# Performance work log

Hardware: AMD Instinct MI355X
Metric: run time of the kernel (lower is better)

The kernel has to match this reference:

```python
import jax, jax.numpy as jnp
import numpy as np

N_LIG, M_POC = 16384, 32768
E_LIG, E_POC, K_CROSS = 163840, 327680, 8
H = 64
L = 4

silu = jax.nn.silu


def _lin(k, fan_in, fan_out):
    k1, k2 = jax.random.split(k)
    s = 1.0 / np.sqrt(fan_in)
    W = jax.random.uniform(k1, (fan_in, fan_out), jnp.float32, -s, s)
    b = jax.random.uniform(k2, (fan_out,), jnp.float32, -s, s)
    return W, b


def setup_inputs() -> dict:
    key = jax.random.key(0)
    ks = jax.random.split(key, 32)
    inp = {
        'lig_x': jax.random.normal(ks[0], (N_LIG, 3), jnp.float32),
        'lig_h': jax.random.normal(ks[1], (N_LIG, 17), jnp.float32),
        'poc_x': jax.random.normal(ks[2], (M_POC, 3), jnp.float32),
        'poc_h': jax.random.normal(ks[3], (M_POC, 29), jnp.float32),
        'lig_edge_index': jax.random.randint(ks[4], (2, E_LIG), 0, N_LIG, jnp.int32),
        'lig_edge_attr': jax.random.normal(ks[5], (E_LIG, 6), jnp.float32),
        'poc_edge_index': jax.random.randint(ks[6], (2, E_POC), 0, M_POC, jnp.int32),
        'poc_edge_attr': jax.random.normal(ks[7], (E_POC, 16), jnp.float32),
        'cross_edge_index': jnp.stack([
            jax.random.randint(ks[8], (N_LIG * K_CROSS,), 0, M_POC, jnp.int32),
            jax.random.randint(ks[9], (N_LIG * K_CROSS,), 0, N_LIG, jnp.int32)]),
        'cross_edge_attr': jax.random.normal(ks[10], (N_LIG * K_CROSS, 16), jnp.float32),
        't': jax.random.uniform(ks[11], (1,), jnp.float32),
    }
    # embeddings
    inp['lig_emb_W'], inp['lig_emb_b'] = _lin(ks[12], 18, H)
    inp['poc_emb_W'], inp['poc_emb_b'] = _lin(ks[13], 29, H)
    inp['lig_ee_W'], inp['lig_ee_b'] = _lin(ks[14], 6, H)
    inp['poc_ee_W'], inp['poc_ee_b'] = _lin(ks[15], 16, H)
    inp['cross_ee_W'], inp['cross_ee_b'] = _lin(ks[16], 16, H)
    # per-layer params stacked along leading L axis
    def stack(kk, fan_in, fan_out):
        Ws, bs = zip(*[_lin(k, fan_in, fan_out) for k in jax.random.split(kk, L)])
        return jnp.stack(Ws), jnp.stack(bs)
    inp['phi_e_W1'], inp['phi_e_b1'] = stack(ks[17], 2 * H + 1 + H, H)
    inp['phi_e_W2'], inp['phi_e_b2'] = stack(ks[18], H, H)
    inp['phi_x_W1'], inp['phi_x_b1'] = stack(ks[19], H, H)
    inp['phi_x_W2'], inp['phi_x_b2'] = stack(ks[20], H, 1)
    inp['phi_h_W1'], inp['phi_h_b1'] = stack(ks[21], 2 * H, H)
    inp['phi_h_W2'], inp['phi_h_b2'] = stack(ks[22], H, H)
    inp['out_W1'], inp['out_b1'] = _lin(ks[23], H, H)
    inp['out_W2'], inp['out_b2'] = _lin(ks[24], H, 1)
    return inp


def _forward(lig_x, lig_h, poc_x, poc_h, lig_edge_attr, poc_edge_attr,
             cross_edge_attr, t,
             lig_emb_W, lig_emb_b, poc_emb_W, poc_emb_b,
             lig_ee_W, lig_ee_b, poc_ee_W, poc_ee_b, cross_ee_W, cross_ee_b,
             phi_e_W1, phi_e_b1, phi_e_W2, phi_e_b2,
             phi_x_W1, phi_x_b1, phi_x_W2, phi_x_b2,
             phi_h_W1, phi_h_b1, phi_h_W2, phi_h_b2,
             out_W1, out_b1, out_W2, out_b2,
             lig_edge_index, poc_edge_index, cross_edge_index):
    n_lig = lig_h.shape[0]
    n_tot = n_lig + poc_h.shape[0]
    t_feat = jnp.broadcast_to(t.reshape(1, 1), (n_lig, 1))
    h_lig = jnp.concatenate([lig_h, t_feat], -1) @ lig_emb_W + lig_emb_b
    h_poc = poc_h @ poc_emb_W + poc_emb_b
    h = jnp.concatenate([h_lig, h_poc], 0)          # [N, H]
    x = jnp.concatenate([lig_x, poc_x], 0)          # [N, 3]
    src = jnp.concatenate([lig_edge_index[0], poc_edge_index[0] + n_lig,
                           cross_edge_index[0] + n_lig])
    dst = jnp.concatenate([lig_edge_index[1], poc_edge_index[1] + n_lig,
                           cross_edge_index[1]])
    eattr = jnp.concatenate([
        lig_edge_attr @ lig_ee_W + lig_ee_b,
        poc_edge_attr @ poc_ee_W + poc_ee_b,
        cross_edge_attr @ cross_ee_W + cross_ee_b], 0)  # [E, H]
    # True = pocket => coords not updated
    update_mask = jnp.concatenate([
        jnp.ones((n_lig, 1), h.dtype), jnp.zeros((n_tot - n_lig, 1), h.dtype)], 0)
    for i in range(phi_e_W1.shape[0]):
        diff = x[src] - x[dst]                                    # [E, 3]
        dist = jnp.sum(diff * diff, -1, keepdims=True) / 100.0    # [E, 1]
        e_in = jnp.concatenate([h[src], h[dst], dist, eattr], -1) # [E, 2H+1+H]
        m = silu(silu(e_in @ phi_e_W1[i] + phi_e_b1[i]) @ phi_e_W2[i] + phi_e_b2[i])
        cw = jnp.tanh(silu(m @ phi_x_W1[i] + phi_x_b1[i]) @ phi_x_W2[i] + phi_x_b2[i])
        coord_agg = jax.ops.segment_sum(diff * cw, dst, num_segments=n_tot) * update_mask
        msg_agg = jax.ops.segment_sum(m, dst, num_segments=n_tot)
        h = h + silu(jnp.concatenate([h, msg_agg], -1) @ phi_h_W1[i] + phi_h_b1[i]) @ phi_h_W2[i] + phi_h_b2[i]
        x = x + coord_agg
    disp = x[:n_lig] - lig_x
    scale = silu(h[:n_lig] @ out_W1 + out_b1) @ out_W2 + out_b2
    return scale * disp


def reference(lig_x, lig_h, poc_x, poc_h, lig_edge_attr, poc_edge_attr,
              cross_edge_attr, t,
              lig_emb_W, lig_emb_b, poc_emb_W, poc_emb_b,
              lig_ee_W, lig_ee_b, poc_ee_W, poc_ee_b, cross_ee_W, cross_ee_b,
              phi_e_W1, phi_e_b1, phi_e_W2, phi_e_b2,
              phi_x_W1, phi_x_b1, phi_x_W2, phi_x_b2,
              phi_h_W1, phi_h_b1, phi_h_W2, phi_h_b2,
              out_W1, out_b1, out_W2, out_b2,
              lig_edge_index, poc_edge_index, cross_edge_index):
    return _forward(lig_x, lig_h, poc_x, poc_h, lig_edge_attr, poc_edge_attr,
                    cross_edge_attr, t,
                    lig_emb_W, lig_emb_b, poc_emb_W, poc_emb_b,
                    lig_ee_W, lig_ee_b, poc_ee_W, poc_ee_b, cross_ee_W, cross_ee_b,
                    phi_e_W1, phi_e_b1, phi_e_W2, phi_e_b2,
                    phi_x_W1, phi_x_b1, phi_x_W2, phi_x_b2,
                    phi_h_W1, phi_h_b1, phi_h_W2, phi_h_b2,
                    out_W1, out_b1, out_W2, out_b2,
                    lig_edge_index, poc_edge_index, cross_edge_index)
```

## Files before the change

### kernel.cpp

```cpp
#include <hip/hip_runtime.h>

#define N_LIG 16384
#define M_POC 32768
#define N_TOT (N_LIG + M_POC)
#define E_LIG 163840
#define E_POC 327680
#define E_CROSS (N_LIG * 8)
#define E_TOT (E_LIG + E_POC + E_CROSS)
#define TE 16

typedef __bf16 bf16_t;
typedef bf16_t bf16x8 __attribute__((ext_vector_type(8)));
typedef bf16_t bf16x4 __attribute__((ext_vector_type(4)));
typedef bf16_t bf16x2 __attribute__((ext_vector_type(2)));
typedef float f32x4 __attribute__((ext_vector_type(4)));

#define S1 168
#define S2 72
#define WAVE_BYTES 7936

__device__ __forceinline__ float silu_f(float v) { return v / (1.0f + __expf(-v)); }

__device__ __forceinline__ float tanh_f(float v) {
    float a = fabsf(v);
    float t = __expf(-2.0f * a);
    float r = (1.0f - t) / (1.0f + t);
    return copysignf(r, v);
}

__device__ __forceinline__ void atomic_add_f32(float* p, float v) {
    __hip_atomic_fetch_add(p, v, __ATOMIC_RELAXED, __HIP_MEMORY_SCOPE_AGENT);
}


__global__ void k_build_edges(const int* __restrict__ lig_ei, const int* __restrict__ poc_ei,
                              const int* __restrict__ cross_ei,
                              int* __restrict__ srcA, int* __restrict__ dstA,
                              int* __restrict__ cnt) {
    int e = blockIdx.x * blockDim.x + threadIdx.x;
    if (e < N_TOT) cnt[e] = 0;
    if (e >= E_TOT) return;
    int s, d;
    if (e < E_LIG) {
        s = lig_ei[e];
        d = lig_ei[E_LIG + e];
    } else if (e < E_LIG + E_POC) {
        int i = e - E_LIG;
        s = poc_ei[i] + N_LIG;
        d = poc_ei[E_POC + i] + N_LIG;
    } else {
        int i = e - E_LIG - E_POC;
        s = cross_ei[i] + N_LIG;
        d = cross_ei[E_CROSS + i];
    }
    srcA[e] = s;
    dstA[e] = d;
}

__global__ void k_hist(const int* __restrict__ dstA, int* __restrict__ cnt) {
    int e = blockIdx.x * blockDim.x + threadIdx.x;
    if (e < E_TOT) atomicAdd(&cnt[dstA[e]], 1);
}

__global__ __launch_bounds__(1024) void k_scan(const int* __restrict__ cnt,
                                               int* __restrict__ rowptr,
                                               int* __restrict__ cursor) {
    __shared__ int sums[1024];
    int tid = threadIdx.x;
    int local[48];
    int s = 0;
    for (int i = 0; i < 48; ++i) { local[i] = s; s += cnt[tid * 48 + i]; }
    sums[tid] = s;
    __syncthreads();
    for (int off = 1; off < 1024; off <<= 1) {
        int v = (tid >= off) ? sums[tid - off] : 0;
        __syncthreads();
        sums[tid] += v;
        __syncthreads();
    }
    int base = (tid == 0) ? 0 : sums[tid - 1];
    for (int i = 0; i < 48; ++i) {
        int v = base + local[i];
        int idx = tid * 48 + i;
        rowptr[idx] = v;
        cursor[idx] = v;
    }
    if (tid == 1023) rowptr[N_TOT] = sums[1023];
}

__global__ void k_scatter(const int* __restrict__ dstA, int* __restrict__ cursor,
                          int* __restrict__ sortedPos) {
    int e = blockIdx.x * blockDim.x + threadIdx.x;
    if (e < E_TOT) sortedPos[e] = atomicAdd(&cursor[dstA[e]], 1);
}

#define PK_G1   (12 * 5 * 4 * 64)
#define PK_G23  (4 * 4 * 4 * 64)
#define PK_WP   (4 * 48 * 256)
#define PK_BEFF (12 * 64)
#define PK_TOT  (PK_G1 + PK_G23 + PK_WP + PK_BEFF)

__global__ void k_pack_all(const float* __restrict__ phi_e_W1, const float* __restrict__ phi_e_b1,
                           const float* __restrict__ lig_ee_W, const float* __restrict__ lig_ee_b,
                           const float* __restrict__ poc_ee_W, const float* __restrict__ poc_ee_b,
                           const float* __restrict__ cross_ee_W, const float* __restrict__ cross_ee_b,
                           const float* __restrict__ phi_e_W2, const float* __restrict__ phi_x_W1,
                           const float* __restrict__ phi_h_W1, const float* __restrict__ phi_h_W2,
                           bf16_t* __restrict__ Bg1, bf16_t* __restrict__ Bg23,
                           float* __restrict__ Wp, float* __restrict__ beff) {
    int tid = blockIdx.x * blockDim.x + threadIdx.x;
    if (tid < PK_G1) {
        int lt = tid / 1280;
        int rem = tid - lt * 1280;
        int c = rem >> 8;
        int nt = (rem >> 6) & 3;
        int lane = rem & 63;
        int l = lt / 3, t = lt % 3;
        const float* W1l = phi_e_W1 + l * 193 * 64;
        const float* We; int K;
        if (t == 0) { We = lig_ee_W; K = 6; }
        else if (t == 1) { We = poc_ee_W; K = 16; }
        else { We = cross_ee_W; K = 16; }
        int col = nt * 16 + (lane & 15);
        int k0 = c * 32 + (lane >> 4) * 8;
        #pragma unroll
        for (int j = 0; j < 8; ++j) {
            int row = k0 + j;
            float v = 0.0f;
            if (row < 129) v = W1l[row * 64 + col];
            else if (row >= 132 && row < 132 + K) {
                int kk = row - 132;
                float a = 0.0f;
                for (int q = 0; q < 64; ++q) a = fmaf(We[kk * 64 + q], W1l[(129 + q) * 64 + col], a);
                v = a;
            }
            Bg1[(size_t)tid * 8 + j] = (bf16_t)v;
        }
    } else if (tid < PK_G1 + PK_G23) {
        int u = tid - PK_G1;
        int lane = u & 63;
        int nt = (u >> 6) & 3;
        int c = (u >> 8) & 3;
        int l = u >> 10;
        const float* W = (c < 2) ? (phi_e_W2 + l * 4096) : (phi_x_W1 + l * 4096);
        int kb = (c & 1) * 32;
        int col = nt * 16 + (lane & 15);
        int k0 = kb + (lane >> 4) * 8;
        #pragma unroll
        for (int j = 0; j < 8; ++j)
            Bg23[(size_t)u * 8 + j] = (bf16_t)W[(k0 + j) * 64 + col];
    } else if (tid < PK_G1 + PK_G23 + PK_WP) {
        int idx = tid - PK_G1 - PK_G23;
        int l = idx / (48 * 256);
        int rem = idx - l * (48 * 256);
        int c = rem / 256;
        int q = rem - c * 256;
        int j = q >> 2;
        int kk = q & 3;
        const float* W; int Ksrc; int k4;
        if (c < 32) { W = phi_h_W1 + l * 128 * 64; Ksrc = 128; k4 = c; }
        else        { W = phi_h_W2 + l * 64 * 64;  Ksrc = 64;  k4 = c - 32; }
        int k = k4 * 4 + kk;
        Wp[idx] = (k < Ksrc) ? W[k * 64 + j] : 0.0f;
    } else if (tid < PK_TOT) {
        int u = tid - PK_G1 - PK_G23 - PK_WP;
        int j = u & 63;
        int lt = u >> 6;
        int l = lt / 3, t = lt % 3;
        const float* W1l = phi_e_W1 + l * 193 * 64;
        const float* Be = (t == 0) ? lig_ee_b : ((t == 1) ? poc_ee_b : cross_ee_b);
        float v = phi_e_b1[l * 64 + j];
        for (int q = 0; q < 64; ++q) v = fmaf(Be[q], W1l[(129 + q) * 64 + j], v);
        beff[u] = v;
    }
}

__global__ void k_embed(const float* __restrict__ lig_x, const float* __restrict__ lig_h,
                        const float* __restrict__ poc_x, const float* __restrict__ poc_h,
                        const float* __restrict__ t,
                        const float* __restrict__ ligW, const float* __restrict__ ligB,
                        const float* __restrict__ pocW, const float* __restrict__ pocB,
                        float* __restrict__ h, bf16_t* __restrict__ hB, float* __restrict__ x) {
    int gid = blockIdx.x * blockDim.x + threadIdx.x;
    int n = gid >> 6;
    int lane = gid & 63;
    if (n >= N_TOT) return;
    float a;
    if (n < N_LIG) {
        a = ligB[lane];
        #pragma unroll
        for (int k = 0; k < 17; ++k) a = fmaf(lig_h[n * 17 + k], ligW[k * 64 + lane], a);
        a = fmaf(t[0], ligW[17 * 64 + lane], a);
        if (lane < 3) x[n * 3 + lane] = lig_x[n * 3 + lane];
    } else {
        int p = n - N_LIG;
        a = pocB[lane];
        #pragma unroll
        for (int k = 0; k < 29; ++k) a = fmaf(poc_h[p * 29 + k], pocW[k * 64 + lane], a);
        if (lane < 3) x[n * 3 + lane] = poc_x[p * 3 + lane];
    }
    h[n * 64 + lane] = a;
    hB[n * 64 + lane] = (bf16_t)a;
}

__global__ __launch_bounds__(256) void k_edge_mfma(
    const bf16_t* __restrict__ hB, const float* __restrict__ x,
    const int* __restrict__ srcA, const int* __restrict__ dstA,
    const int* __restrict__ sortedPos,
    const float* __restrict__ lig_attr, const float* __restrict__ poc_attr,
    const float* __restrict__ cross_attr,
    const bf16_t* __restrict__ Bg1L,
    const float* __restrict__ beffL,
    const bf16_t* __restrict__ Bg23L,
    const float* __restrict__ b2, const float* __restrict__ bx1,
    const float* __restrict__ Wx2, const float* __restrict__ bx2,
    bf16_t* __restrict__ mBuf, float* __restrict__ coord_agg) {
    __shared__ __align__(16) char lds[4 * WAVE_BYTES];
    const int lane = threadIdx.x & 63;
    const int wave = threadIdx.x >> 6;
    bf16_t* einA = (bf16_t*)(lds + wave * WAVE_BYTES);
    bf16_t* mA   = (bf16_t*)(lds + wave * WAVE_BYTES + 5376);
    float*  dfL  = (float*)(lds + wave * WAVE_BYTES + 5376 + 2304);
    const int base = (blockIdx.x * 4 + wave) * TE;

    int t; const float* attrBase;
    if (base < E_LIG) { t = 0; attrBase = lig_attr + (size_t)base * 6; }
    else if (base < E_LIG + E_POC) { t = 1; attrBase = poc_attr + (size_t)(base - E_LIG) * 16; }
    else { t = 2; attrBase = cross_attr + (size_t)(base - E_LIG - E_POC) * 16; }

    const int e16 = base + (lane & 15);
    const int sv = srcA[e16];
    const int dv = dstA[e16];
    const int sp = sortedPos[e16];

    {
        bf16x8 z = {(bf16_t)0.f, (bf16_t)0.f, (bf16_t)0.f, (bf16_t)0.f,
                    (bf16_t)0.f, (bf16_t)0.f, (bf16_t)0.f, (bf16_t)0.f};
        *(bf16x8*)(einA + (lane >> 2) * S1 + 128 + (lane & 3) * 8) = z;
    }

    #pragma unroll
    for (int i = 0; i < 4; ++i) {
        const int row = i * 4 + (lane >> 4);
        const int s = __shfl(sv, row, 64);
        const int d = __shfl(dv, row, 64);
        bf16x4 hs = *(const bf16x4*)(hB + (size_t)s * 64 + (lane & 15) * 4);
        bf16x4 hd = *(const bf16x4*)(hB + (size_t)d * 64 + (lane & 15) * 4);
        *(bf16x4*)(einA + row * S1 + (lane & 15) * 4) = hs;
        *(bf16x4*)(einA + row * S1 + 64 + (lane & 15) * 4) = hd;
    }

    if (lane < 16) {
        const float* xs = x + (size_t)sv * 3;
        const float* xd = x + (size_t)dv * 3;
        float d0 = xs[0] - xd[0];
        float d1 = xs[1] - xd[1];
        float d2 = xs[2] - xd[2];
        float dist = (d0 * d0 + d1 * d1 + d2 * d2) * 0.01f;
        einA[lane * S1 + 128] = (bf16_t)dist;
        *(float4*)(dfL + lane * 4) = (float4){d0, d1, d2, dist};
    }

    {
        const int r = lane >> 2, q = lane & 3;
        if (t == 0) {
            if (q < 3) {
                float2 a = *(const float2*)(attrBase + r * 6 + q * 2);
                bf16x2 av = {(bf16_t)a.x, (bf16_t)a.y};
                *(bf16x2*)(einA + r * S1 + 132 + q * 2) = av;
            }
        } else {
            float4 a = *(const float4*)(attrBase + r * 16 + q * 4);
            bf16x4 av = {(bf16_t)a.x, (bf16_t)a.y, (bf16_t)a.z, (bf16_t)a.w};
            *(bf16x4*)(einA + r * S1 + 132 + q * 4) = av;
        }
    }
    __syncthreads();

    const int mcol = lane & 15;
    const int mrow0 = (lane >> 4) * 4;
    const int kgrp = lane >> 4;

    const bf16_t* Bg1 = Bg1L + (size_t)t * 5 * 4 * 512;
    const float* beff = beffL + t * 64;
    f32x4 acc1[4];
    #pragma unroll
    for (int nt = 0; nt < 4; ++nt) {
        float bv = beff[nt * 16 + mcol];
        acc1[nt] = (f32x4){bv, bv, bv, bv};
    }
    const bf16_t* aBase = einA + mcol * S1 + kgrp * 8;
    #pragma unroll
    for (int c = 0; c < 5; ++c) {
        bf16x8 af = *(const bf16x8*)(aBase + c * 32);
        #pragma unroll
        for (int nt = 0; nt < 4; ++nt) {
            bf16x8 bfr = *(const bf16x8*)(Bg1 + ((size_t)(c * 4 + nt) * 64 + lane) * 8);
            acc1[nt] = __builtin_amdgcn_mfma_f32_16x16x32_bf16(af, bfr, acc1[nt], 0, 0, 0);
        }
    }
    __syncthreads();
    #pragma unroll
    for (int nt = 0; nt < 4; ++nt)
        #pragma unroll
        for (int g = 0; g < 4; ++g)
            mA[(mrow0 + g) * S2 + nt * 16 + mcol] = (bf16_t)silu_f(acc1[nt][g]);
    __syncthreads();

    f32x4 acc2[4];
    #pragma unroll
    for (int nt = 0; nt < 4; ++nt) {
        float bv = b2[nt * 16 + mcol];
        acc2[nt] = (f32x4){bv, bv, bv, bv};
    }
    const bf16_t* aBase2 = mA + mcol * S2 + kgrp * 8;
    #pragma unroll
    for (int c = 0; c < 2; ++c) {
        bf16x8 af = *(const bf16x8*)(aBase2 + c * 32);
        #pragma unroll
        for (int nt = 0; nt < 4; ++nt) {
            bf16x8 bfr = *(const bf16x8*)(Bg23L + ((size_t)(c * 4 + nt) * 64 + lane) * 8);
            acc2[nt] = __builtin_amdgcn_mfma_f32_16x16x32_bf16(af, bfr, acc2[nt], 0, 0, 0);
        }
    }
    __syncthreads();
    #pragma unroll
    for (int nt = 0; nt < 4; ++nt)
        #pragma unroll
        for (int g = 0; g < 4; ++g)
            mA[(mrow0 + g) * S2 + nt * 16 + mcol] = (bf16_t)silu_f(acc2[nt][g]);
    __syncthreads();

    #pragma unroll
    for (int p = 0; p < 2; ++p) {
        const int r = p * 8 + (lane >> 3);
        const int c8 = (lane & 7) * 8;
        bf16x8 mrow = *(const bf16x8*)(mA + r * S2 + c8);
        const int pos = __shfl(sp, r, 64);
        *(bf16x8*)(mBuf + (size_t)pos * 64 + c8) = mrow;
    }

    f32x4 acc3[4];
    #pragma unroll
    for (int nt = 0; nt < 4; ++nt) {
        float bv = bx1[nt * 16 + mcol];
        acc3[nt] = (f32x4){bv, bv, bv, bv};
    }
    const bf16_t* Bg3 = Bg23L + (size_t)2 * 4 * 512;
    #pragma unroll
    for (int c = 0; c < 2; ++c) {
        bf16x8 af = *(const bf16x8*)(aBase2 + c * 32);
        #pragma unroll
        for (int nt = 0; nt < 4; ++nt) {
            bf16x8 bfr = *(const bf16x8*)(Bg3 + ((size_t)(c * 4 + nt) * 64 + lane) * 8);
            acc3[nt] = __builtin_amdgcn_mfma_f32_16x16x32_bf16(af, bfr, acc3[nt], 0, 0, 0);
        }
    }

    const float bx2v = bx2[0];
    float s[4] = {0.f, 0.f, 0.f, 0.f};
    #pragma unroll
    for (int nt = 0; nt < 4; ++nt) {
        float w = Wx2[nt * 16 + mcol];
        #pragma unroll
        for (int g = 0; g < 4; ++g) s[g] = fmaf(silu_f(acc3[nt][g]), w, s[g]);
    }
    #pragma unroll
    for (int g = 0; g < 4; ++g) {
        float p = s[g];
        #pragma unroll
        for (int off = 1; off < 16; off <<= 1) p += __shfl_xor(p, off, 64);
        const float cw = tanh_f(p + bx2v);
        const int d = __shfl(dv, mrow0 + g, 64);
        if (d < N_LIG && mcol < 3)
            atomic_add_f32(&coord_agg[d * 3 + mcol], dfL[(mrow0 + g) * 4 + mcol] * cw);
    }
}

__global__ __launch_bounds__(256) void k_node(
    float* __restrict__ h, bf16_t* __restrict__ hB, float* __restrict__ x,
    const bf16_t* __restrict__ mBuf, const int* __restrict__ rowptr,
    float* __restrict__ coord,
    const float* __restrict__ Wh1p, const float* __restrict__ bh1,
    const float* __restrict__ Wh2p, const float* __restrict__ bh2) {
    __shared__ __align__(16) float lds[4][TE * 128];
    const int lane = threadIdx.x & 63;
    const int wave = threadIdx.x >> 6;
    float* inL = lds[wave];
    const int base = (blockIdx.x * 4 + wave) * TE;

    #pragma unroll
    for (int i = 0; i < 4; ++i) {
        int fidx = i * 256 + lane * 4;
        float4 v = *(const float4*)(h + (size_t)base * 64 + fidx);
        *(float4*)(inL + (fidx >> 6) * 128 + (fidx & 63)) = v;
    }

    const int n16 = base + (lane & 15);
    const int rp0 = rowptr[n16];
    const int rp1 = rowptr[n16 + 1];
    const int sub = lane >> 4;
    const int f4 = (lane & 15) * 4;
    for (int r = 0; r < TE; ++r) {
        const int s0 = __shfl(rp0, r, 64);
        const int s1 = __shfl(rp1, r, 64);
        float a0 = 0.f, a1 = 0.f, a2 = 0.f, a3 = 0.f;
        for (int i = s0 + sub; i < s1; i += 4) {
            bf16x4 v = *(const bf16x4*)(mBuf + (size_t)i * 64 + f4);
            a0 += (float)v[0]; a1 += (float)v[1]; a2 += (float)v[2]; a3 += (float)v[3];
        }
        a0 += __shfl_xor(a0, 16, 64); a1 += __shfl_xor(a1, 16, 64);
        a2 += __shfl_xor(a2, 16, 64); a3 += __shfl_xor(a3, 16, 64);
        a0 += __shfl_xor(a0, 32, 64); a1 += __shfl_xor(a1, 32, 64);
        a2 += __shfl_xor(a2, 32, 64); a3 += __shfl_xor(a3, 32, 64);
        if (lane < 16)
            *(float4*)(inL + r * 128 + 64 + f4) = (float4){a0, a1, a2, a3};
    }
    __syncthreads();

    float acc[TE];
    #pragma unroll
    for (int r = 0; r < TE; ++r) acc[r] = bh1[lane];
    for (int c = 0; c < 32; ++c) {
        const float4 w = *(const float4*)(Wh1p + (c * 64 + lane) * 4);
        #pragma unroll
        for (int r = 0; r < TE; ++r) {
            const float4 v = *(const float4*)(inL + r * 128 + c * 4);
            acc[r] = fmaf(v.x, w.x, fmaf(v.y, w.y, fmaf(v.z, w.z, fmaf(v.w, w.w, acc[r]))));
        }
    }
    __syncthreads();
    #pragma unroll
    for (int r = 0; r < TE; ++r) inL[r * 64 + lane] = silu_f(acc[r]);
    __syncthreads();

    float acc2[TE];
    #pragma unroll
    for (int r = 0; r < TE; ++r) acc2[r] = bh2[lane];
    for (int c = 0; c < 16; ++c) {
        const float4 w = *(const float4*)(Wh2p + (c * 64 + lane) * 4);
        #pragma unroll
        for (int r = 0; r < TE; ++r) {
            const float4 v = *(const float4*)(inL + r * 64 + c * 4);
            acc2[r] = fmaf(v.x, w.x, fmaf(v.y, w.y, fmaf(v.z, w.z, fmaf(v.w, w.w, acc2[r]))));
        }
    }
    for (int r = 0; r < TE; ++r) {
        const int n = base + r;
        float hv = h[n * 64 + lane] + acc2[r];
        h[n * 64 + lane] = hv;
        hB[n * 64 + lane] = (bf16_t)hv;
        if (lane < 3) {
            if (n < N_LIG) x[n * 3 + lane] += coord[n * 3 + lane];
            coord[n * 3 + lane] = 0.0f;
        }
    }
}

__global__ void k_out(const float* __restrict__ h, const float* __restrict__ x,
                      const float* __restrict__ lig_x,
                      const float* __restrict__ oW1, const float* __restrict__ ob1,
                      const float* __restrict__ oW2, const float* __restrict__ ob2,
                      float* __restrict__ out) {
    int gid = blockIdx.x * blockDim.x + threadIdx.x;
    int n = gid >> 6;
    int lane = gid & 63;
    if (n >= N_LIG) return;
    float hv = h[n * 64 + lane];
    float a = ob1[lane];
    #pragma unroll
    for (int k = 0; k < 64; ++k) a = fmaf(__shfl(hv, k, 64), oW1[k * 64 + lane], a);
    float p = silu_f(a) * oW2[lane];
    #pragma unroll
    for (int off = 32; off > 0; off >>= 1) p += __shfl_xor(p, off, 64);
    float scale = p + ob2[0];
    if (lane < 3) out[n * 3 + lane] = scale * (x[n * 3 + lane] - lig_x[n * 3 + lane]);
}

extern "C" void kernel_launch(void* const* d_in, const int* in_sizes, int n_in,
                              void* d_out, int out_size, void* d_ws, size_t ws_size,
                              hipStream_t stream) {
    const float* lig_x      = (const float*)d_in[0];
    const float* lig_h      = (const float*)d_in[1];
    const float* poc_x      = (const float*)d_in[2];
    const float* poc_h      = (const float*)d_in[3];
    const int*   lig_ei     = (const int*)d_in[4];
    const float* lig_attr   = (const float*)d_in[5];
    const int*   poc_ei     = (const int*)d_in[6];
    const float* poc_attr   = (const float*)d_in[7];
    const int*   cross_ei   = (const int*)d_in[8];
    const float* cross_attr = (const float*)d_in[9];
    const float* t          = (const float*)d_in[10];
    const float* lig_emb_W  = (const float*)d_in[11];
    const float* lig_emb_b  = (const float*)d_in[12];
    const float* poc_emb_W  = (const float*)d_in[13];
    const float* poc_emb_b  = (const float*)d_in[14];
    const float* lig_ee_W   = (const float*)d_in[15];
    const float* lig_ee_b   = (const float*)d_in[16];
    const float* poc_ee_W   = (const float*)d_in[17];
    const float* poc_ee_b   = (const float*)d_in[18];
    const float* cross_ee_W = (const float*)d_in[19];
    const float* cross_ee_b = (const float*)d_in[20];
    const float* phi_e_W1   = (const float*)d_in[21];
    const float* phi_e_b1   = (const float*)d_in[22];
    const float* phi_e_W2   = (const float*)d_in[23];
    const float* phi_e_b2   = (const float*)d_in[24];
    const float* phi_x_W1   = (const float*)d_in[25];
    const float* phi_x_b1   = (const float*)d_in[26];
    const float* phi_x_W2   = (const float*)d_in[27];
    const float* phi_x_b2   = (const float*)d_in[28];
    const float* phi_h_W1   = (const float*)d_in[29];
    const float* phi_h_b1   = (const float*)d_in[30];
    const float* phi_h_W2   = (const float*)d_in[31];
    const float* phi_h_b2   = (const float*)d_in[32];
    const float* out_W1     = (const float*)d_in[33];
    const float* out_b1     = (const float*)d_in[34];
    const float* out_W2     = (const float*)d_in[35];
    const float* out_b2     = (const float*)d_in[36];

    char* p = (char*)d_ws;
    auto carve = [&](size_t bytes) { char* r = p; p += (bytes + 255) & ~(size_t)255; return r; };
    float*  h      = (float*)carve((size_t)N_TOT * 64 * 4);
    bf16_t* hB     = (bf16_t*)carve((size_t)N_TOT * 64 * 2);
    float*  xx     = (float*)carve((size_t)N_TOT * 3 * 4);
    float*  coord  = (float*)carve((size_t)N_TOT * 3 * 4);
    float*  Wp     = (float*)carve((size_t)4 * 48 * 256 * 4);
    float*  beff   = (float*)carve((size_t)12 * 64 * 4);
    bf16_t* Bg1    = (bf16_t*)carve((size_t)12 * 5 * 4 * 512 * 2);
    bf16_t* Bg23   = (bf16_t*)carve((size_t)4 * 16 * 512 * 2);
    int*    srcA   = (int*)carve((size_t)E_TOT * 4);
    int*    dstA   = (int*)carve((size_t)E_TOT * 4);
    int*    sortedPos = (int*)carve((size_t)E_TOT * 4);
    int*    cnt    = (int*)carve((size_t)N_TOT * 4);
    int*    cursor = (int*)carve((size_t)N_TOT * 4);
    int*    rowptr = (int*)carve((size_t)(N_TOT + 1) * 4);
    bf16_t* mBuf   = (bf16_t*)carve((size_t)E_TOT * 64 * 2);

    k_build_edges<<<E_TOT / 256, 256, 0, stream>>>(lig_ei, poc_ei, cross_ei, srcA, dstA, cnt);
    k_hist<<<E_TOT / 256, 256, 0, stream>>>(dstA, cnt);
    k_scan<<<1, 1024, 0, stream>>>(cnt, rowptr, cursor);
    k_scatter<<<E_TOT / 256, 256, 0, stream>>>(dstA, cursor, sortedPos);
    k_pack_all<<<(PK_TOT + 255) / 256, 256, 0, stream>>>(
        phi_e_W1, phi_e_b1, lig_ee_W, lig_ee_b, poc_ee_W, poc_ee_b, cross_ee_W, cross_ee_b,
        phi_e_W2, phi_x_W1, phi_h_W1, phi_h_W2, Bg1, Bg23, Wp, beff);
    k_embed<<<(N_TOT * 64) / 256, 256, 0, stream>>>(
        lig_x, lig_h, poc_x, poc_h, t, lig_emb_W, lig_emb_b, poc_emb_W, poc_emb_b, h, hB, xx);
    hipMemsetAsync(coord, 0, (size_t)N_TOT * 3 * 4, stream);

    for (int l = 0; l < 4; ++l) {
        k_edge_mfma<<<E_TOT / 64, 256, 0, stream>>>(
            hB, xx, srcA, dstA, sortedPos, lig_attr, poc_attr, cross_attr,
            Bg1 + (size_t)l * 3 * 5 * 4 * 512, beff + (size_t)l * 3 * 64,
            Bg23 + (size_t)l * 16 * 512,
            phi_e_b2 + l * 64, phi_x_b1 + l * 64,
            phi_x_W2 + l * 64, phi_x_b2 + l,
            mBuf, coord);
        k_node<<<N_TOT / 64, 256, 0, stream>>>(
            h, hB, xx, mBuf, rowptr, coord,
            Wp + (size_t)l * 48 * 256, phi_h_b1 + l * 64,
            Wp + (size_t)l * 48 * 256 + 32 * 256, phi_h_b2 + l * 64);
    }

    k_out<<<(N_LIG * 64) / 256, 256, 0, stream>>>(
        h, xx, lig_x, out_W1, out_b1, out_W2, out_b2, (float*)d_out);
}
```

Measured before the change: 865.2 us.

## Load node features straight into MFMA registers and shrink edge kernel LDS

The edge kernel now loads each edge's source and destination bf16 features directly into the MFMA A-fragment registers instead of staging them through shared memory. Only the edge attributes and distance (repacked into a compact 16+1 K-slot layout, with the W1 packing reordered to match) go through LDS. Block-wide barriers are replaced by per-wave lgkmcnt waits, since each wave uses only its own LDS region. Coordinates are padded to float4 so they load in one vector read, and launch bounds request higher occupancy. The trade-off is more gather traffic per lane and reliance on wave-local LDS ordering, which is correct only if no cross-wave sharing exists.

```diff
diff --git a/kernel.cpp b/kernel.cpp
--- a/kernel.cpp
+++ b/kernel.cpp
@@ -15,9 +15,8 @@
 typedef bf16_t bf16x2 __attribute__((ext_vector_type(2)));
 typedef float f32x4 __attribute__((ext_vector_type(4)));
 
-#define S1 168
 #define S2 72
-#define WAVE_BYTES 7936
+#define WAVE_BYTES (1792 + 2304 + 256)
 
 __device__ __forceinline__ float silu_f(float v) { return v / (1.0f + __expf(-v)); }
 
@@ -30,6 +29,10 @@
 
 __device__ __forceinline__ void atomic_add_f32(float* p, float v) {
     __hip_atomic_fetch_add(p, v, __ATOMIC_RELAXED, __HIP_MEMORY_SCOPE_AGENT);
+}
+
+__device__ __forceinline__ void lds_fence() {
+    asm volatile("s_waitcnt lgkmcnt(0)" ::: "memory");
 }
 
 
@@ -127,12 +130,16 @@
         for (int j = 0; j < 8; ++j) {
             int row = k0 + j;
             float v = 0.0f;
-            if (row < 129) v = W1l[row * 64 + col];
-            else if (row >= 132 && row < 132 + K) {
-                int kk = row - 132;
-                float a = 0.0f;
-                for (int q = 0; q < 64; ++q) a = fmaf(We[kk * 64 + q], W1l[(129 + q) * 64 + col], a);
-                v = a;
+            if (row < 128) v = W1l[row * 64 + col];
+            else if (row < 144) {
+                int kk = row - 128;
+                if (kk < K) {
+                    float a = 0.0f;
+                    for (int q = 0; q < 64; ++q) a = fmaf(We[kk * 64 + q], W1l[(129 + q) * 64 + col], a);
+                    v = a;
+                }
+            } else if (row == 144) {
+                v = W1l[128 * 64 + col];
             }
             Bg1[(size_t)tid * 8 + j] = (bf16_t)v;
         }
@@ -180,7 +187,7 @@
                         const float* __restrict__ t,
                         const float* __restrict__ ligW, const float* __restrict__ ligB,
                         const float* __restrict__ pocW, const float* __restrict__ pocB,
-                        float* __restrict__ h, bf16_t* __restrict__ hB, float* __restrict__ x) {
+                        float* __restrict__ h, bf16_t* __restrict__ hB, float* __restrict__ x4) {
     int gid = blockIdx.x * blockDim.x + threadIdx.x;
     int n = gid >> 6;
     int lane = gid & 63;
@@ -191,20 +198,20 @@
         #pragma unroll
         for (int k = 0; k < 17; ++k) a = fmaf(lig_h[n * 17 + k], ligW[k * 64 + lane], a);
         a = fmaf(t[0], ligW[17 * 64 + lane], a);
-        if (lane < 3) x[n * 3 + lane] = lig_x[n * 3 + lane];
+        if (lane < 4) x4[n * 4 + lane] = (lane < 3) ? lig_x[n * 3 + lane] : 0.0f;
     } else {
         int p = n - N_LIG;
         a = pocB[lane];
         #pragma unroll
         for (int k = 0; k < 29; ++k) a = fmaf(poc_h[p * 29 + k], pocW[k * 64 + lane], a);
-        if (lane < 3) x[n * 3 + lane] = poc_x[p * 3 + lane];
+        if (lane < 4) x4[n * 4 + lane] = (lane < 3) ? poc_x[p * 3 + lane] : 0.0f;
     }
     h[n * 64 + lane] = a;
     hB[n * 64 + lane] = (bf16_t)a;
 }
 
-__global__ __launch_bounds__(256) void k_edge_mfma(
-    const bf16_t* __restrict__ hB, const float* __restrict__ x,
+__global__ __launch_bounds__(256, 6) void k_edge_mfma(
+    const bf16_t* __restrict__ hB, const float* __restrict__ x4,
     const int* __restrict__ srcA, const int* __restrict__ dstA,
     const int* __restrict__ sortedPos,
     const float* __restrict__ lig_attr, const float* __restrict__ poc_attr,
@@ -218,94 +225,92 @@
     __shared__ __align__(16) char lds[4 * WAVE_BYTES];
     const int lane = threadIdx.x & 63;
     const int wave = threadIdx.x >> 6;
-    bf16_t* einA = (bf16_t*)(lds + wave * WAVE_BYTES);
-    bf16_t* mA   = (bf16_t*)(lds + wave * WAVE_BYTES + 5376);
-    float*  dfL  = (float*)(lds + wave * WAVE_BYTES + 5376 + 2304);
+    bf16_t* exL = (bf16_t*)(lds + wave * WAVE_BYTES);
+    bf16_t* mA  = (bf16_t*)(lds + wave * WAVE_BYTES + 1792);
+    float*  dfL = (float*)(lds + wave * WAVE_BYTES + 1792 + 2304);
     const int base = (blockIdx.x * 4 + wave) * TE;
 
-    int t; const float* attrBase;
-    if (base < E_LIG) { t = 0; attrBase = lig_attr + (size_t)base * 6; }
-    else if (base < E_LIG + E_POC) { t = 1; attrBase = poc_attr + (size_t)(base - E_LIG) * 16; }
-    else { t = 2; attrBase = cross_attr + (size_t)(base - E_LIG - E_POC) * 16; }
+    int tt; const float* attrBase; int astride;
+    if (base < E_LIG) { tt = 0; attrBase = lig_attr + (size_t)base * 6; astride = 6; }
+    else if (base < E_LIG + E_POC) { tt = 1; attrBase = poc_attr + (size_t)(base - E_LIG) * 16; astride = 16; }
+    else { tt = 2; attrBase = cross_attr + (size_t)(base - E_LIG - E_POC) * 16; astride = 16; }
 
     const int e16 = base + (lane & 15);
     const int sv = srcA[e16];
     const int dv = dstA[e16];
     const int sp = sortedPos[e16];
 
+    const int mcol = lane & 15;
+    const int kgrp = lane >> 4;
+    const int mrow0 = kgrp * 4;
+
+    bf16x8 af0 = *(const bf16x8*)(hB + (size_t)sv * 64 + kgrp * 8);
+    bf16x8 af1 = *(const bf16x8*)(hB + (size_t)sv * 64 + 32 + kgrp * 8);
+    bf16x8 af2 = *(const bf16x8*)(hB + (size_t)dv * 64 + kgrp * 8);
+    bf16x8 af3 = *(const bf16x8*)(hB + (size_t)dv * 64 + 32 + kgrp * 8);
+
     {
         bf16x8 z = {(bf16_t)0.f, (bf16_t)0.f, (bf16_t)0.f, (bf16_t)0.f,
                     (bf16_t)0.f, (bf16_t)0.f, (bf16_t)0.f, (bf16_t)0.f};
-        *(bf16x8*)(einA + (lane >> 2) * S1 + 128 + (lane & 3) * 8) = z;
-    }
-
-    #pragma unroll
-    for (int i = 0; i < 4; ++i) {
-        const int row = i * 4 + (lane >> 4);
-        const int s = __shfl(sv, row, 64);
-        const int d = __shfl(dv, row, 64);
-        bf16x4 hs = *(const bf16x4*)(hB + (size_t)s * 64 + (lane & 15) * 4);
-        bf16x4 hd = *(const bf16x4*)(hB + (size_t)d * 64 + (lane & 15) * 4);
-        *(bf16x4*)(einA + row * S1 + (lane & 15) * 4) = hs;
-        *(bf16x4*)(einA + row * S1 + 64 + (lane & 15) * 4) = hd;
-    }
-
+        *(bf16x8*)(exL + (lane >> 2) * 56 + (lane & 3) * 8) = z;
+    }
+    lds_fence();
     if (lane < 16) {
-        const float* xs = x + (size_t)sv * 3;
-        const float* xd = x + (size_t)dv * 3;
-        float d0 = xs[0] - xd[0];
-        float d1 = xs[1] - xd[1];
-        float d2 = xs[2] - xd[2];
+        float4 xs = *(const float4*)(x4 + (size_t)sv * 4);
+        float4 xd = *(const float4*)(x4 + (size_t)dv * 4);
+        float d0 = xs.x - xd.x;
+        float d1 = xs.y - xd.y;
+        float d2 = xs.z - xd.z;
         float dist = (d0 * d0 + d1 * d1 + d2 * d2) * 0.01f;
-        einA[lane * S1 + 128] = (bf16_t)dist;
+        exL[lane * 56 + 16] = (bf16_t)dist;
         *(float4*)(dfL + lane * 4) = (float4){d0, d1, d2, dist};
-    }
-
-    {
-        const int r = lane >> 2, q = lane & 3;
-        if (t == 0) {
-            if (q < 3) {
-                float2 a = *(const float2*)(attrBase + r * 6 + q * 2);
-                bf16x2 av = {(bf16_t)a.x, (bf16_t)a.y};
-                *(bf16x2*)(einA + r * S1 + 132 + q * 2) = av;
-            }
+        const float* attr = attrBase + lane * astride;
+        if (tt == 0) {
+            float2 a0 = *(const float2*)(attr);
+            float2 a1 = *(const float2*)(attr + 2);
+            float2 a2 = *(const float2*)(attr + 4);
+            bf16x8 w0 = {(bf16_t)a0.x, (bf16_t)a0.y, (bf16_t)a1.x, (bf16_t)a1.y,
+                         (bf16_t)a2.x, (bf16_t)a2.y, (bf16_t)0.f, (bf16_t)0.f};
+            *(bf16x8*)(exL + lane * 56) = w0;
         } else {
-            float4 a = *(const float4*)(attrBase + r * 16 + q * 4);
-            bf16x4 av = {(bf16_t)a.x, (bf16_t)a.y, (bf16_t)a.z, (bf16_t)a.w};
-            *(bf16x4*)(einA + r * S1 + 132 + q * 4) = av;
-        }
-    }
-    __syncthreads();
-
-    const int mcol = lane & 15;
-    const int mrow0 = (lane >> 4) * 4;
-    const int kgrp = lane >> 4;
-
-    const bf16_t* Bg1 = Bg1L + (size_t)t * 5 * 4 * 512;
-    const float* beff = beffL + t * 64;
+            float4 a0 = *(const float4*)(attr);
+            float4 a1 = *(const float4*)(attr + 4);
+            float4 a2 = *(const float4*)(attr + 8);
+            float4 a3 = *(const float4*)(attr + 12);
+            bf16x8 w0 = {(bf16_t)a0.x, (bf16_t)a0.y, (bf16_t)a0.z, (bf16_t)a0.w,
+                         (bf16_t)a1.x, (bf16_t)a1.y, (bf16_t)a1.z, (bf16_t)a1.w};
+            bf16x8 w1 = {(bf16_t)a2.x, (bf16_t)a2.y, (bf16_t)a2.z, (bf16_t)a2.w,
+                         (bf16_t)a3.x, (bf16_t)a3.y, (bf16_t)a3.z, (bf16_t)a3.w};
+            *(bf16x8*)(exL + lane * 56) = w0;
+            *(bf16x8*)(exL + lane * 56 + 8) = w1;
+        }
+    }
+    lds_fence();
+
+    const bf16_t* Bg1 = Bg1L + (size_t)tt * 5 * 4 * 512;
+    const float* beff = beffL + tt * 64;
     f32x4 acc1[4];
     #pragma unroll
     for (int nt = 0; nt < 4; ++nt) {
         float bv = beff[nt * 16 + mcol];
         acc1[nt] = (f32x4){bv, bv, bv, bv};
     }
-    const bf16_t* aBase = einA + mcol * S1 + kgrp * 8;
+    bf16x8 af4 = *(const bf16x8*)(exL + mcol * 56 + kgrp * 8);
+    bf16x8 afs[5] = {af0, af1, af2, af3, af4};
     #pragma unroll
     for (int c = 0; c < 5; ++c) {
-        bf16x8 af = *(const bf16x8*)(aBase + c * 32);
         #pragma unroll
         for (int nt = 0; nt < 4; ++nt) {
             bf16x8 bfr = *(const bf16x8*)(Bg1 + ((size_t)(c * 4 + nt) * 64 + lane) * 8);
-            acc1[nt] = __builtin_amdgcn_mfma_f32_16x16x32_bf16(af, bfr, acc1[nt], 0, 0, 0);
-        }
-    }
-    __syncthreads();
+            acc1[nt] = __builtin_amdgcn_mfma_f32_16x16x32_bf16(afs[c], bfr, acc1[nt], 0, 0, 0);
+        }
+    }
     #pragma unroll
     for (int nt = 0; nt < 4; ++nt)
         #pragma unroll
         for (int g = 0; g < 4; ++g)
             mA[(mrow0 + g) * S2 + nt * 16 + mcol] = (bf16_t)silu_f(acc1[nt][g]);
-    __syncthreads();
+    lds_fence();
 
     f32x4 acc2[4];
     #pragma unroll
@@ -323,13 +328,13 @@
             acc2[nt] = __builtin_amdgcn_mfma_f32_16x16x32_bf16(af, bfr, acc2[nt], 0, 0, 0);
         }
     }
-    __syncthreads();
+    lds_fence();
     #pragma unroll
     for (int nt = 0; nt < 4; ++nt)
         #pragma unroll
         for (int g = 0; g < 4; ++g)
             mA[(mrow0 + g) * S2 + nt * 16 + mcol] = (bf16_t)silu_f(acc2[nt][g]);
-    __syncthreads();
+    lds_fence();
 
     #pragma unroll
     for (int p = 0; p < 2; ++p) {
@@ -378,7 +383,7 @@
 }
 
 __global__ __launch_bounds__(256) void k_node(
-    float* __restrict__ h, bf16_t* __restrict__ hB, float* __restrict__ x,
+    float* __restrict__ h, bf16_t* __restrict__ hB, float* __restrict__ x4,
     const bf16_t* __restrict__ mBuf, const int* __restrict__ rowptr,
     float* __restrict__ coord,
     const float* __restrict__ Wh1p, const float* __restrict__ bh1,
@@ -451,13 +456,13 @@
         h[n * 64 + lane] = hv;
         hB[n * 64 + lane] = (bf16_t)hv;
         if (lane < 3) {
-            if (n < N_LIG) x[n * 3 + lane] += coord[n * 3 + lane];
+            if (n < N_LIG) x4[n * 4 + lane] += coord[n * 3 + lane];
             coord[n * 3 + lane] = 0.0f;
         }
     }
 }
 
-__global__ void k_out(const float* __restrict__ h, const float* __restrict__ x,
+__global__ void k_out(const float* __restrict__ h, const float* __restrict__ x4,
                       const float* __restrict__ lig_x,
                       const float* __restrict__ oW1, const float* __restrict__ ob1,
                       const float* __restrict__ oW2, const float* __restrict__ ob2,
@@ -474,7 +479,7 @@
     #pragma unroll
     for (int off = 32; off > 0; off >>= 1) p += __shfl_xor(p, off, 64);
     float scale = p + ob2[0];
-    if (lane < 3) out[n * 3 + lane] = scale * (x[n * 3 + lane] - lig_x[n * 3 + lane]);
+    if (lane < 3) out[n * 3 + lane] = scale * (x4[n * 4 + lane] - lig_x[n * 3 + lane]);
 }
 
 extern "C" void kernel_launch(void* const* d_in, const int* in_sizes, int n_in,
@@ -522,7 +527,7 @@
     auto carve = [&](size_t bytes) { char* r = p; p += (bytes + 255) & ~(size_t)255; return r; };
     float*  h      = (float*)carve((size_t)N_TOT * 64 * 4);
     bf16_t* hB     = (bf16_t*)carve((size_t)N_TOT * 64 * 2);
-    float*  xx     = (float*)carve((size_t)N_TOT * 3 * 4);
+    float*  x4     = (float*)carve((size_t)N_TOT * 4 * 4);
     float*  coord  = (float*)carve((size_t)N_TOT * 3 * 4);
     float*  Wp     = (float*)carve((size_t)4 * 48 * 256 * 4);
     float*  beff   = (float*)carve((size_t)12 * 64 * 4);
@@ -544,23 +549,23 @@
         phi_e_W1, phi_e_b1, lig_ee_W, lig_ee_b, poc_ee_W, poc_ee_b, cross_ee_W, cross_ee_b,
         phi_e_W2, phi_x_W1, phi_h_W1, phi_h_W2, Bg1, Bg23, Wp, beff);
     k_embed<<<(N_TOT * 64) / 256, 256, 0, stream>>>(
-        lig_x, lig_h, poc_x, poc_h, t, lig_emb_W, lig_emb_b, poc_emb_W, poc_emb_b, h, hB, xx);
+        lig_x, lig_h, poc_x, poc_h, t, lig_emb_W, lig_emb_b, poc_emb_W, poc_emb_b, h, hB, x4);
     hipMemsetAsync(coord, 0, (size_t)N_TOT * 3 * 4, stream);
 
     for (int l = 0; l < 4; ++l) {
         k_edge_mfma<<<E_TOT / 64, 256, 0, stream>>>(
-            hB, xx, srcA, dstA, sortedPos, lig_attr, poc_attr, cross_attr,
+            hB, x4, srcA, dstA, sortedPos, lig_attr, poc_attr, cross_attr,
             Bg1 + (size_t)l * 3 * 5 * 4 * 512, beff + (size_t)l * 3 * 64,
             Bg23 + (size_t)l * 16 * 512,
             phi_e_b2 + l * 64, phi_x_b1 + l * 64,
             phi_x_W2 + l * 64, phi_x_b2 + l,
             mBuf, coord);
         k_node<<<N_TOT / 64, 256, 0, stream>>>(
-            h, hB, xx, mBuf, rowptr, coord,
+            h, hB, x4, mBuf, rowptr, coord,
             Wp + (size_t)l * 48 * 256, phi_h_b1 + l * 64,
             Wp + (size_t)l * 48 * 256 + 32 * 256, phi_h_b2 + l * 64);
     }
 
     k_out<<<(N_LIG * 64) / 256, 256, 0, stream>>>(
-        h, xx, lig_x, out_W1, out_b1, out_W2, out_b2, (float*)d_out);
-}
+        h, x4, lig_x, out_W1, out_b1, out_W2, out_b2, (float*)d_out);
+}
```

New measurement: 888.1 us. 1.03x slower.
